# Kernel optimization log

Hardware: AMD Instinct MI355X
Metric: run time of the kernel (lower is better)

## Reference

```python
import jax, jax.numpy as jnp
import numpy as np

EPS_NORM = 1e-12  # F.normalize eps
EPS_LOG = 1e-8    # forward's default eps


def setup_inputs() -> dict:
    key = jax.random.key(0)
    x = jax.random.normal(key, (16384, 256), dtype=jnp.float32)
    return {"student_output": x}


def reference(student_output) -> jnp.ndarray:
    x = student_output
    # L2-normalize rows (F.normalize with p=2, eps=1e-12)
    norm = jnp.maximum(jnp.linalg.norm(x, axis=-1, keepdims=True), EPS_NORM)
    xn = x / norm
    # pairwise squared euclidean via gram: ||xi-xj||^2 = 2 - 2<xi,xj> for unit vectors
    gram = xn @ xn.T  # [B, B]
    sq = jnp.clip(2.0 - 2.0 * gram, 0.0)
    b = sq.shape[0]
    eye = jnp.eye(b, dtype=bool)
    # mask diagonal before sqrt (avoids 0-grad/nan issues) then set to +inf
    dist = jnp.sqrt(jnp.where(eye, 1.0, sq))
    dist = jnp.where(eye, jnp.inf, dist)
    min_dist = jnp.min(dist, axis=1)  # [B] distance to nearest neighbor
    loss = -jnp.mean(jnp.log(min_dist + EPS_LOG))
    return loss
```

## Files before the change

kernel.cpp:

```cpp
#include <hip/hip_runtime.h>
#include <hip/hip_bf16.h>
#include <math.h>


typedef __attribute__((ext_vector_type(8))) short bf16x8;
typedef __attribute__((ext_vector_type(16))) float f32x16;

#define NROWS 16384
#define NDIM  256
#define NBLK  256
#define UNITS_PER 33

__global__ __launch_bounds__(256) void knorm(const float* __restrict__ x,
                                             float* __restrict__ rn) {
    int wid = threadIdx.x >> 6, lane = threadIdx.x & 63;
    int row = blockIdx.x * 4 + wid;
    const float4* xr = (const float4*)(x + (size_t)row * NDIM);
    float4 v = xr[lane];
    float ss = v.x * v.x + v.y * v.y + v.z * v.z + v.w * v.w;
    #pragma unroll
    for (int m = 1; m < 64; m <<= 1) ss += __shfl_xor(ss, m, 64);
    if (lane == 0) rn[row] = 1.0f / fmaxf(sqrtf(ss), 1e-12f);
}

__device__ inline unsigned bf_rne(float f) {
    union { float f; unsigned u; } c; c.f = f;
    return (c.u + 0x7FFFu + ((c.u >> 16) & 1u)) >> 16;
}
__device__ inline unsigned pack2(float lo, float hi) {
    return bf_rne(lo) | (bf_rne(hi) << 16);
}

__global__ __launch_bounds__(256) void kpack(const float* __restrict__ x,
                                             const float* __restrict__ rn,
                                             uint4* __restrict__ F) {
    int g = blockIdx.x * 256 + threadIdx.x;
    int t32  = g >> 10;
    int rem  = g & 1023;
    int ks   = rem >> 6;
    int lane = rem & 63;
    int row  = t32 * 32 + (lane & 31);
    int kb   = ks * 16 + (lane >> 5) * 8;
    float s = rn[row];
    const float4* xr = (const float4*)(x + (size_t)row * NDIM + kb);
    float4 a = xr[0], b = xr[1];
    uint4 o;
    o.x = pack2(a.x * s, a.y * s);
    o.y = pack2(a.z * s, a.w * s);
    o.z = pack2(b.x * s, b.y * s);
    o.w = pack2(b.z * s, b.w * s);
    F[g] = o;
}

__device__ inline void stage16(const uint4* __restrict__ g, const uint4* l) {
    __builtin_amdgcn_global_load_lds(
        (const __attribute__((address_space(1))) unsigned*)g,
        (__attribute__((address_space(3))) unsigned*)l, 16, 0, 0);
}

__device__ inline unsigned fkey(float f) {
    unsigned u = __builtin_bit_cast(unsigned, f);
    return (u & 0x80000000u) ? ~u : (u | 0x80000000u);
}

template<int CTRL>
__device__ inline float dpp_rot(float x) {
    int xi = __builtin_bit_cast(int, x);
    int yi = __builtin_amdgcn_update_dpp(xi, xi, CTRL, 0xF, 0xF, false);
    return __builtin_bit_cast(float, yi);
}

__global__ __launch_bounds__(512, 2) void kmax(const bf16x8* __restrict__ F,
                                               unsigned* __restrict__ rowcand) {
    __shared__ uint4 sbuf[3][1024];
    __shared__ uint4 dump[64];

    const int tid  = threadIdx.x;
    const int wid  = tid >> 6;
    const int lane = tid & 63;
    const int L    = lane & 31;
    const int hi   = lane >> 5;
    const uint4* F4 = (const uint4*)F;

    const int b  = ((blockIdx.x & 7) << 5) | (blockIdx.x >> 3);
    const int u0 = b * UNITS_PER;

    int cib = 0;
    while ((cib + 1) * (520 - 8 * (cib + 1)) <= u0) ++cib;
    int cjt = 16 * cib + (u0 - cib * (520 - 8 * cib));

    int myit = cib * 16 + wid * 2;
    bf16x8 bfr0[16], bfr1[16];
    #pragma unroll
    for (int ks = 0; ks < 16; ++ks) {
        bfr0[ks] = F[(myit + 0) * 1024 + ks * 64 + lane];
        bfr1[ks] = F[(myit + 1) * 1024 + ks * 64 + lane];
    }

    auto stage_unit = [&](int jt, uint4* dst) {
        const uint4* gp = F4 + (size_t)jt * 1024;
        stage16(gp + tid,       dst + wid * 64);
        stage16(gp + 512 + tid, dst + 512 + wid * 64);
    };
    auto stepc = [](int& ib, int& jt) {
        if (++jt == 512) { if (ib < 31) { ++ib; jt = 16 * ib; } else jt = 511; }
    };

    int sib = cib, sjt = cjt;
    stage_unit(sjt, sbuf[0]);
    stage16(F4 + tid, dump);
    stepc(sib, sjt);
    stage_unit(sjt, sbuf[1]);

    float rm0[16], rm1[16];
    #pragma unroll
    for (int r = 0; r < 16; ++r) { rm0[r] = -1e30f; rm1[r] = -1e30f; }

    const bool dvalid = (((L >> 2) & 1) == hi);
    const int  dreg   = (L & 3) | ((L >> 3) << 2);

    auto flush_i = [&](int fib) {
        #pragma unroll
        for (int r = 0; r < 16; ++r) {
            float a = rm0[r];
            a = fmaxf(a, dpp_rot<0x121>(a));
            a = fmaxf(a, dpp_rot<0x122>(a));
            a = fmaxf(a, dpp_rot<0x124>(a));
            a = fmaxf(a, dpp_rot<0x128>(a));
            rm0[r] = fmaxf(a, __shfl_xor(a, 16, 64));
            float c = rm1[r];
            c = fmaxf(c, dpp_rot<0x121>(c));
            c = fmaxf(c, dpp_rot<0x122>(c));
            c = fmaxf(c, dpp_rot<0x124>(c));
            c = fmaxf(c, dpp_rot<0x128>(c));
            rm1[r] = fmaxf(c, __shfl_xor(c, 16, 64));
        }
        float v0 = rm0[0], v1 = rm1[0];
        #pragma unroll
        for (int r = 1; r < 16; ++r) {
            v0 = (dreg == r) ? rm0[r] : v0;
            v1 = (dreg == r) ? rm1[r] : v1;
        }
        if (dvalid) {
            int base = fib * 512 + wid * 64;
            atomicMax(&rowcand[base + L],      fkey(v0));
            atomicMax(&rowcand[base + 32 + L], fkey(v1));
        }
    };

    int myib = cib;
    int bsel = 0;
    for (int s = 0; s < UNITS_PER; ++s) {
        asm volatile("s_waitcnt vmcnt(3)" ::: "memory");
        __builtin_amdgcn_s_barrier();
        __builtin_amdgcn_sched_barrier(0);

        const uint4* sb = &sbuf[bsel][0];
        f32x16 c0 = {0.f}, c1 = {0.f};
        #pragma unroll
        for (int ks = 0; ks < 16; ++ks) {
            bf16x8 af = *(const bf16x8*)(sb + ks * 64 + lane);
            c0 = __builtin_amdgcn_mfma_f32_32x32x16_bf16(bfr0[ks], af, c0, 0, 0, 0);
            c1 = __builtin_amdgcn_mfma_f32_32x32x16_bf16(bfr1[ks], af, c1, 0, 0, 0);
        }

        const bool m0 = (cjt == myit), m1 = (cjt == myit + 1);
        float jm = -1e30f;
        #pragma unroll
        for (int r = 0; r < 16; ++r) {
            float v0 = c0[r], v1 = c1[r];
            if (m0 && dvalid && r == dreg) v0 = -1e30f;
            if (m1 && dvalid && r == dreg) v1 = -1e30f;
            rm0[r] = fmaxf(rm0[r], v0);
            rm1[r] = fmaxf(rm1[r], v1);
            jm = fmaxf(jm, fmaxf(v0, v1));
        }
        jm = fmaxf(jm, __shfl_xor(jm, 32, 64));
        if (lane < 32) atomicMax(&rowcand[cjt * 32 + L], fkey(jm));

        stepc(cib, cjt);
        if (cib != myib) {
            flush_i(myib);
            #pragma unroll
            for (int r = 0; r < 16; ++r) { rm0[r] = -1e30f; rm1[r] = -1e30f; }
            myib = cib;
            if (s + 1 < UNITS_PER) {
                myit = cib * 16 + wid * 2;
                #pragma unroll
                for (int ks = 0; ks < 16; ++ks) {
                    bfr0[ks] = F[(myit + 0) * 1024 + ks * 64 + lane];
                    bfr1[ks] = F[(myit + 1) * 1024 + ks * 64 + lane];
                }
            }
        }

        __builtin_amdgcn_sched_barrier(0);
        stepc(sib, sjt);
        stage_unit(sjt, &sbuf[bsel + 2 >= 3 ? bsel - 1 : bsel + 2][0]);
        bsel = (bsel + 1 >= 3) ? 0 : bsel + 1;
    }
    flush_i(myib);
}

__global__ __launch_bounds__(256) void kloss1(const unsigned* __restrict__ rowcand,
                                              float* __restrict__ partial) {
    int i = blockIdx.x * 256 + threadIdx.x;
    unsigned k = rowcand[i];
    unsigned u = (k & 0x80000000u) ? (k ^ 0x80000000u) : ~k;
    float gv = __builtin_bit_cast(float, u);
    float d = sqrtf(fmaxf(2.f - 2.f * gv, 0.f));
    float acc = logf(d + 1e-8f);
    #pragma unroll
    for (int m = 1; m < 64; m <<= 1) acc += __shfl_xor(acc, m, 64);
    __shared__ float p[4];
    int wid = threadIdx.x >> 6, lane = threadIdx.x & 63;
    if (lane == 0) p[wid] = acc;
    __syncthreads();
    if (threadIdx.x == 0)
        partial[blockIdx.x] = (p[0] + p[1]) + (p[2] + p[3]);
}

__global__ __launch_bounds__(64) void kloss2(const float* __restrict__ partial,
                                             float* __restrict__ out) {
    float acc = partial[threadIdx.x];
    #pragma unroll
    for (int m = 1; m < 64; m <<= 1) acc += __shfl_xor(acc, m, 64);
    if (threadIdx.x == 0) out[0] = -acc / (float)NROWS;
}

extern "C" void kernel_launch(void* const* d_in, const int* in_sizes, int n_in,
                              void* d_out, int out_size, void* d_ws, size_t ws_size,
                              hipStream_t stream) {
    const float* x = (const float*)d_in[0];
    float* out = (float*)d_out;
    char* ws = (char*)d_ws;

    uint4*    F       = (uint4*)ws;
    float*    rn      = (float*)(ws + 8u * 1024u * 1024u);
    unsigned* rowcand = (unsigned*)(ws + 8u * 1024u * 1024u + 65536u);
    float*    partial = (float*)(ws + 8u * 1024u * 1024u + 131072u);

    hipMemsetAsync(rowcand, 0, NROWS * sizeof(unsigned), stream);
    knorm<<<NROWS / 4, 256, 0, stream>>>(x, rn);
    kpack<<<(NROWS * NDIM / 8) / 256, 256, 0, stream>>>(x, rn, F);
    kmax <<<NBLK, 512, 0, stream>>>((const bf16x8*)F, rowcand);
    kloss1<<<64, 256, 0, stream>>>(rowcand, partial);
    kloss2<<<1, 64, 0, stream>>>(partial, out);
}
```

Before: 94.50 us.

## Split symmetric gram work into 512 blocks of 256 threads with finer row tiles

Each row block in kmax now covers 256 rows (4 waves of 64) instead of 512. The grid doubles to 512 blocks of 256 threads, and units are spread evenly with a fractional 32.5-per-block split. The triangular schedule, staging loop and flush indexing are rewritten to match. The diagonal-masking compare is moved into a branch that only runs on diagonal tiles, and the column max is split into two accumulators to shorten the dependency chain. The intent is better load balance and occupancy across CUs, at the cost of more B-fragment reloads and more atomics per useful work.

```diff
diff --git a/kernel.cpp b/kernel.cpp
--- a/kernel.cpp
+++ b/kernel.cpp
@@ -8,8 +8,7 @@
 
 #define NROWS 16384
 #define NDIM  256
-#define NBLK  256
-#define UNITS_PER 33
+#define NBLK  512
 
 __global__ __launch_bounds__(256) void knorm(const float* __restrict__ x,
                                              float* __restrict__ rn) {
@@ -70,7 +69,7 @@
     return __builtin_bit_cast(float, yi);
 }
 
-__global__ __launch_bounds__(512, 2) void kmax(const bf16x8* __restrict__ F,
+__global__ __launch_bounds__(256, 2) void kmax(const bf16x8* __restrict__ F,
                                                unsigned* __restrict__ rowcand) {
     __shared__ uint4 sbuf[3][1024];
     __shared__ uint4 dump[64];
@@ -82,14 +81,15 @@
     const int hi   = lane >> 5;
     const uint4* F4 = (const uint4*)F;
 
-    const int b  = ((blockIdx.x & 7) << 5) | (blockIdx.x >> 3);
-    const int u0 = b * UNITS_PER;
+    const int b  = ((blockIdx.x & 7) << 6) | (blockIdx.x >> 3);
+    const int u0   = (b * 65) >> 1;
+    const int uend = ((b + 1) * 65) >> 1;
 
     int cib = 0;
-    while ((cib + 1) * (520 - 8 * (cib + 1)) <= u0) ++cib;
-    int cjt = 16 * cib + (u0 - cib * (520 - 8 * cib));
-
-    int myit = cib * 16 + wid * 2;
+    while ((cib + 1) * (516 - 4 * (cib + 1)) <= u0) ++cib;
+    int cjt = 8 * cib + (u0 - cib * (516 - 4 * cib));
+
+    int myit = cib * 8 + wid * 2;
     bf16x8 bfr0[16], bfr1[16];
     #pragma unroll
     for (int ks = 0; ks < 16; ++ks) {
@@ -99,11 +99,12 @@
 
     auto stage_unit = [&](int jt, uint4* dst) {
         const uint4* gp = F4 + (size_t)jt * 1024;
-        stage16(gp + tid,       dst + wid * 64);
-        stage16(gp + 512 + tid, dst + 512 + wid * 64);
+        #pragma unroll
+        for (int q = 0; q < 4; ++q)
+            stage16(gp + q * 256 + tid, dst + q * 256 + wid * 64);
     };
     auto stepc = [](int& ib, int& jt) {
-        if (++jt == 512) { if (ib < 31) { ++ib; jt = 16 * ib; } else jt = 511; }
+        if (++jt == 512) { if (ib < 63) { ++ib; jt = 8 * ib; } else jt = 511; }
     };
 
     int sib = cib, sjt = cjt;
@@ -142,7 +143,7 @@
             v1 = (dreg == r) ? rm1[r] : v1;
         }
         if (dvalid) {
-            int base = fib * 512 + wid * 64;
+            int base = fib * 256 + wid * 64;
             atomicMax(&rowcand[base + L],      fkey(v0));
             atomicMax(&rowcand[base + 32 + L], fkey(v1));
         }
@@ -150,8 +151,8 @@
 
     int myib = cib;
     int bsel = 0;
-    for (int s = 0; s < UNITS_PER; ++s) {
-        asm volatile("s_waitcnt vmcnt(3)" ::: "memory");
+    for (int s = u0; s < uend; ++s) {
+        asm volatile("s_waitcnt vmcnt(5)" ::: "memory");
         __builtin_amdgcn_s_barrier();
         __builtin_amdgcn_sched_barrier(0);
 
@@ -164,17 +165,30 @@
             c1 = __builtin_amdgcn_mfma_f32_32x32x16_bf16(bfr1[ks], af, c1, 0, 0, 0);
         }
 
-        const bool m0 = (cjt == myit), m1 = (cjt == myit + 1);
-        float jm = -1e30f;
-        #pragma unroll
-        for (int r = 0; r < 16; ++r) {
-            float v0 = c0[r], v1 = c1[r];
-            if (m0 && dvalid && r == dreg) v0 = -1e30f;
-            if (m1 && dvalid && r == dreg) v1 = -1e30f;
-            rm0[r] = fmaxf(rm0[r], v0);
-            rm1[r] = fmaxf(rm1[r], v1);
-            jm = fmaxf(jm, fmaxf(v0, v1));
-        }
+        float jma = -1e30f, jmb = -1e30f;
+        if (cjt == myit || cjt == myit + 1) {
+            const bool m0 = (cjt == myit);
+            #pragma unroll
+            for (int r = 0; r < 16; ++r) {
+                float v0 = c0[r], v1 = c1[r];
+                if (m0 && dvalid && r == dreg)  v0 = -1e30f;
+                if (!m0 && dvalid && r == dreg) v1 = -1e30f;
+                rm0[r] = fmaxf(rm0[r], v0);
+                rm1[r] = fmaxf(rm1[r], v1);
+                if (r & 1) jmb = fmaxf(jmb, fmaxf(v0, v1));
+                else       jma = fmaxf(jma, fmaxf(v0, v1));
+            }
+        } else {
+            #pragma unroll
+            for (int r = 0; r < 16; ++r) {
+                float v0 = c0[r], v1 = c1[r];
+                rm0[r] = fmaxf(rm0[r], v0);
+                rm1[r] = fmaxf(rm1[r], v1);
+                if (r & 1) jmb = fmaxf(jmb, fmaxf(v0, v1));
+                else       jma = fmaxf(jma, fmaxf(v0, v1));
+            }
+        }
+        float jm = fmaxf(jma, jmb);
         jm = fmaxf(jm, __shfl_xor(jm, 32, 64));
         if (lane < 32) atomicMax(&rowcand[cjt * 32 + L], fkey(jm));
 
@@ -184,8 +198,8 @@
             #pragma unroll
             for (int r = 0; r < 16; ++r) { rm0[r] = -1e30f; rm1[r] = -1e30f; }
             myib = cib;
-            if (s + 1 < UNITS_PER) {
-                myit = cib * 16 + wid * 2;
+            if (s + 1 < uend) {
+                myit = cib * 8 + wid * 2;
                 #pragma unroll
                 for (int ks = 0; ks < 16; ++ks) {
                     bfr0[ks] = F[(myit + 0) * 1024 + ks * 64 + lane];
@@ -243,7 +257,7 @@
     hipMemsetAsync(rowcand, 0, NROWS * sizeof(unsigned), stream);
     knorm<<<NROWS / 4, 256, 0, stream>>>(x, rn);
     kpack<<<(NROWS * NDIM / 8) / 256, 256, 0, stream>>>(x, rn, F);
-    kmax <<<NBLK, 512, 0, stream>>>((const bf16x8*)F, rowcand);
+    kmax <<<NBLK, 256, 0, stream>>>((const bf16x8*)F, rowcand);
     kloss1<<<64, 256, 0, stream>>>(rowcand, partial);
     kloss2<<<1, 64, 0, stream>>>(partial, out);
 }
```

Result: no change. 93.47 us (-1.1%).
